# Optimization experiments

Hardware: AMD Instinct MI355X
Metric: run time of the kernel (lower is better)

## Reference

```python
import jax, jax.numpy as jnp
import numpy as np

DIM = 384
HEADS = 12
WS = 7
MLPH = 1536
B = 32
EPS = 1e-5


def _rel_index():
    coords = np.stack(np.meshgrid(np.arange(WS), np.arange(WS), indexing='ij'))  # [2,7,7]
    cf = coords.reshape(2, -1)  # [2,49]
    rel = cf[:, :, None] - cf[:, None, :]  # [2,49,49]
    rel = rel.transpose(1, 2, 0).astype(np.int64)
    rel[:, :, 0] += WS - 1
    rel[:, :, 1] += WS - 1
    rel[:, :, 0] *= 2 * WS - 1
    return jnp.asarray(rel.sum(-1), dtype=jnp.int32)  # [49,49]


def setup_inputs() -> dict:
    key = jax.random.key(0)
    ks = jax.random.split(key, 16)
    H, W = 56, 56
    L = H * W
    s = 0.02
    inp = {
        'x': jax.random.normal(ks[0], (B, L, DIM), jnp.float32),
        'ln1_g': jnp.ones((DIM,), jnp.float32),
        'ln1_b': jnp.zeros((DIM,), jnp.float32),
        'qkv_w': jax.random.normal(ks[1], (DIM, 3 * DIM), jnp.float32) * s,
        'qkv_b': jnp.zeros((3 * DIM,), jnp.float32),
        'rpb_table': jax.random.normal(ks[2], ((2 * WS - 1) ** 2, HEADS), jnp.float32) * s,
        'proj_w': jax.random.normal(ks[3], (DIM, DIM), jnp.float32) * s,
        'proj_b': jnp.zeros((DIM,), jnp.float32),
        'ln2_g': jnp.ones((DIM,), jnp.float32),
        'ln2_b': jnp.zeros((DIM,), jnp.float32),
        'mlp_w1': jax.random.normal(ks[4], (DIM, MLPH), jnp.float32) * s,
        'mlp_b1': jnp.zeros((MLPH,), jnp.float32),
        'mlp_w2': jax.random.normal(ks[5], (MLPH, DIM), jnp.float32) * s,
        'mlp_b2': jnp.zeros((DIM,), jnp.float32),
        'rel_idx': _rel_index(),
        'H': H,
        'W': W,
    }
    return inp


def _ln(x, g, b):
    m = jnp.mean(x, axis=-1, keepdims=True)
    v = jnp.mean(jnp.square(x - m), axis=-1, keepdims=True)
    return (x - m) * jax.lax.rsqrt(v + EPS) * g + b


def reference(x, ln1_g, ln1_b, qkv_w, qkv_b, rpb_table, proj_w, proj_b,
              ln2_g, ln2_b, mlp_w1, mlp_b1, mlp_w2, mlp_b2, rel_idx, H, W):
    Bb, L, C = x.shape
    N = WS * WS
    hd = C // HEADS
    scale = hd ** -0.5

    shortcut = x
    h = _ln(x, ln1_g, ln1_b).reshape(Bb, H, W, C)
    # window partition -> [nW, 49, C]
    h = h.reshape(Bb, H // WS, WS, W // WS, WS, C).transpose(0, 1, 3, 2, 4, 5)
    wins = h.reshape(-1, N, C)
    nW = wins.shape[0]

    qkv = (wins @ qkv_w + qkv_b).reshape(nW, N, 3, HEADS, hd).transpose(2, 0, 3, 1, 4)
    q, k, v = qkv[0] * scale, qkv[1], qkv[2]  # [nW, heads, 49, hd]

    attn = jnp.einsum('bhnd,bhmd->bhnm', q, k)
    bias = rpb_table[rel_idx].transpose(2, 0, 1)  # [heads,49,49]
    attn = jax.nn.softmax(attn + bias[None], axis=-1)
    out = jnp.einsum('bhnm,bhmd->bhnd', attn, v).transpose(0, 2, 1, 3).reshape(nW, N, C)
    out = out @ proj_w + proj_b

    # window reverse -> [B, L, C]
    out = out.reshape(Bb, H // WS, W // WS, WS, WS, C).transpose(0, 1, 3, 2, 4, 5).reshape(Bb, L, C)

    x = shortcut + out
    h2 = _ln(x, ln2_g, ln2_b)
    mlp = jax.nn.gelu(h2 @ mlp_w1 + mlp_b1, approximate=False) @ mlp_w2 + mlp_b2
    return x + mlp
```

## Files before the change

kernel.cpp:

```cpp
#include <hip/hip_runtime.h>
#include <hip/hip_bf16.h>
#include <cstdint>
#include <cstddef>

#define HEADS 12
#define LL 3136
#define ROWS 100352
#define SCALE 0.17677669529663687f

typedef __hip_bfloat16 bf16;
typedef __attribute__((ext_vector_type(8))) short short8;
typedef __attribute__((ext_vector_type(4))) short s4;
typedef __attribute__((ext_vector_type(4))) float f32x4;

__device__ __forceinline__ float bf2f(unsigned short u) {
  union { uint32_t u32; float f; } x; x.u32 = ((uint32_t)u) << 16; return x.f;
}
__device__ __forceinline__ unsigned short f2bf_bits(float f) {
  union { float f; uint32_t u; } x; x.f = f;
  uint32_t r = x.u + 0x7fffu + ((x.u >> 16) & 1u);
  return (unsigned short)(r >> 16);
}

__global__ void prep_transpose(const float* __restrict__ src, bf16* __restrict__ dst,
                               int K, int N, int scaleLim, float scale) {
  int idx = blockIdx.x * 256 + threadIdx.x;
  if (idx >= K * N) return;
  int n = idx / K;
  int k = idx - n * K;
  float v = src[(size_t)k * N + n];
  if (n < scaleLim) v *= scale;
  dst[idx] = __float2bfloat16(v);
}

__global__ void prep_qb(const float* __restrict__ qkv_b, float* __restrict__ qb) {
  int idx = blockIdx.x * 256 + threadIdx.x;
  if (idx < 1152) qb[idx] = qkv_b[idx] * (idx < 384 ? SCALE : 1.0f);
}

__global__ void prep_biasM(const float* __restrict__ rpb, const int* __restrict__ rel,
                           f32x4* __restrict__ biasM) {
  int h = blockIdx.x;
  int t = blockIdx.y;
  int mi = t >> 2, ni = t & 3;
  int lane = threadIdx.x;
  int q = ni * 16 + (lane & 15);
  int g = lane >> 4;
  f32x4 v;
  #pragma unroll
  for (int j = 0; j < 4; ++j) {
    int k = mi * 16 + g * 4 + j;
    float b;
    if (k < 49) b = (q < 49) ? rpb[rel[q * 49 + k] * HEADS + h] : 0.f;
    else        b = -1e30f;
    v[j] = b;
  }
  biasM[((h * 4 + mi) * 4 + ni) * 64 + lane] = v;
}

template<bool WIN>
__global__ __launch_bounds__(256) void ln_kernel(const float* __restrict__ x,
    const float* __restrict__ g, const float* __restrict__ b, bf16* __restrict__ out) {
  int row = blockIdx.x * 4 + (threadIdx.x >> 6);
  int lane = threadIdx.x & 63;
  size_t src;
  if (WIN) {
    int w = row / 49, p = row - w * 49;
    int bb = w >> 6, wy = (w >> 3) & 7, wx = w & 7;
    int iy = p / 7, ix = p - iy * 7;
    int l = (wy * 7 + iy) * 56 + wx * 7 + ix;
    src = ((size_t)bb * LL + l) * 384;
  } else {
    src = (size_t)row * 384;
  }
  const float* xr = x + src;
  float vals[6];
  float s = 0.f, s2 = 0.f;
  #pragma unroll
  for (int j = 0; j < 6; ++j) {
    float v = xr[lane + 64 * j];
    vals[j] = v; s += v; s2 += v * v;
  }
  #pragma unroll
  for (int off = 32; off >= 1; off >>= 1) {
    s  += __shfl_xor(s, off);
    s2 += __shfl_xor(s2, off);
  }
  float m  = s * (1.f / 384.f);
  float var = s2 * (1.f / 384.f) - m * m;
  float rs = rsqrtf(var + 1e-5f);
  bf16* orow = out + (size_t)row * 384;
  #pragma unroll
  for (int j = 0; j < 6; ++j) {
    int c = lane + 64 * j;
    orow[c] = __float2bfloat16((vals[j] - m) * rs * g[c] + b[c]);
  }
}

template<int EPI>
__global__ __launch_bounds__(256) void gemm_bt(const bf16* __restrict__ A,
    const bf16* __restrict__ Bt, const float* __restrict__ bias,
    bf16* __restrict__ Cb, float* __restrict__ Cf, const float* __restrict__ resid,
    int M, int N, int K) {
  __shared__ bf16 lsA[2][128 * 32];
  __shared__ bf16 lsB[2][128 * 32];
  const int t = threadIdx.x;
  const int lane = t & 63;
  const int wave = t >> 6;
  const int wm = wave >> 1, wn = wave & 1;
  const int lrow = lane & 15;
  const int lk = (lane >> 4) * 8;
  const int n0 = blockIdx.x * 128;
  const int m0 = blockIdx.y * 128;

  f32x4 acc[4][4];
  #pragma unroll
  for (int i = 0; i < 4; ++i)
    #pragma unroll
    for (int j = 0; j < 4; ++j) acc[i][j] = (f32x4){0.f, 0.f, 0.f, 0.f};

  auto stage = [&](int buf, int k0) {
    #pragma unroll
    for (int i = 0; i < 2; ++i) {
      int e = (i * 256 + t) * 8;
      int r = e >> 5, c = e & 31;
      const bf16* ga = A  + (size_t)(m0 + r) * K + (k0 + c);
      const bf16* gb = Bt + (size_t)(n0 + r) * K + (k0 + c);
      __builtin_amdgcn_global_load_lds((const __attribute__((address_space(1))) void*)ga,
          (__attribute__((address_space(3))) void*)&lsA[buf][e], 16, 0, 0);
      __builtin_amdgcn_global_load_lds((const __attribute__((address_space(1))) void*)gb,
          (__attribute__((address_space(3))) void*)&lsB[buf][e], 16, 0, 0);
    }
  };

  auto compute = [&](int buf) {
    short8 af[4], bfr[4];
    #pragma unroll
    for (int mi = 0; mi < 4; ++mi)
      af[mi] = *(const short8*)&lsA[buf][(wm * 64 + mi * 16 + lrow) * 32 + lk];
    #pragma unroll
    for (int ni = 0; ni < 4; ++ni)
      bfr[ni] = *(const short8*)&lsB[buf][(wn * 64 + ni * 16 + lrow) * 32 + lk];
    #pragma unroll
    for (int mi = 0; mi < 4; ++mi)
      #pragma unroll
      for (int ni = 0; ni < 4; ++ni)
        acc[mi][ni] = __builtin_amdgcn_mfma_f32_16x16x32_bf16(af[mi], bfr[ni], acc[mi][ni], 0, 0, 0);
  };

  stage(0, 0);
  __syncthreads();
  int cur = 0;
  const int nt = K >> 5;
  for (int it = 0; it < nt - 1; ++it) {
    stage(cur ^ 1, (it + 1) * 32);
    compute(cur);
    __syncthreads();
    cur ^= 1;
  }
  compute(cur);

  #pragma unroll
  for (int mi = 0; mi < 4; ++mi) {
    #pragma unroll
    for (int ni = 0; ni < 4; ++ni) {
      int col = n0 + wn * 64 + ni * 16 + lrow;
      float bv = bias[col];
      #pragma unroll
      for (int j = 0; j < 4; ++j) {
        int row = m0 + wm * 64 + mi * 16 + (lane >> 4) * 4 + j;
        float v = acc[mi][ni][j] + bv;
        if constexpr (EPI == 0) {
          Cb[(size_t)row * N + col] = __float2bfloat16(v);
        } else if constexpr (EPI == 1) {
          v = v * 0.5f * (1.0f + erff(v * 0.70710678118654752f));
          Cb[(size_t)row * N + col] = __float2bfloat16(v);
        } else if constexpr (EPI == 2) {
          int w = row / 49, p = row - w * 49;
          int bb = w >> 6, wy = (w >> 3) & 7, wx = w & 7;
          int iy = p / 7, ix = p - iy * 7;
          int l = (wy * 7 + iy) * 56 + wx * 7 + ix;
          size_t di = ((size_t)bb * LL + l) * 384 + col;
          Cf[di] = v + resid[di];
        } else {
          size_t di = (size_t)row * N + col;
          Cf[di] = v + resid[di];
        }
      }
    }
  }
}

__global__ __launch_bounds__(256) void attn_mfma(const bf16* __restrict__ qkv,
    const f32x4* __restrict__ biasM, bf16* __restrict__ out) {
  __shared__ __align__(16) short lds4[4][6272];
  const int wv = threadIdx.x >> 6;
  const int lane = threadIdx.x & 63;
  const int w = blockIdx.x * 4 + wv;
  const int h = blockIdx.y;
  short* L = &lds4[wv][0];
  const short* base = (const short*)(qkv + (size_t)w * 49 * 1152 + h * 32);

  #pragma unroll
  for (int i = 0; i < 4; ++i) {
    int t = i * 64 + lane;
    int r = t >> 2, c = t & 3;
    short8 qv, kv, vv;
    if (r < 49) {
      const short* rp = base + (size_t)r * 1152;
      qv = *(const short8*)(rp + c * 8);
      kv = *(const short8*)(rp + 384 + c * 8);
      vv = *(const short8*)(rp + 768 + c * 8);
    } else {
      qv = (short8)0; kv = (short8)0; vv = (short8)0;
    }
    *(short8*)&L[r * 32 + c * 8] = kv;
    *(short8*)&L[2048 + r * 32 + c * 8] = qv;
    #pragma unroll
    for (int j = 0; j < 8; ++j) L[4096 + (c * 8 + j) * 68 + r] = vv[j];
  }

  const int g = lane >> 4, r15 = lane & 15;

  short8 ka[4], qb[4];
  #pragma unroll
  for (int mi = 0; mi < 4; ++mi)
    ka[mi] = *(const short8*)&L[(mi * 16 + r15) * 32 + g * 8];
  #pragma unroll
  for (int ni = 0; ni < 4; ++ni)
    qb[ni] = *(const short8*)&L[2048 + (ni * 16 + r15) * 32 + g * 8];

  f32x4 sT[4][4];
  #pragma unroll
  for (int mi = 0; mi < 4; ++mi)
    #pragma unroll
    for (int ni = 0; ni < 4; ++ni)
      sT[mi][ni] = biasM[((h * 4 + mi) * 4 + ni) * 64 + lane];
  #pragma unroll
  for (int mi = 0; mi < 4; ++mi)
    #pragma unroll
    for (int ni = 0; ni < 4; ++ni)
      sT[mi][ni] = __builtin_amdgcn_mfma_f32_16x16x32_bf16(ka[mi], qb[ni], sT[mi][ni], 0, 0, 0);

  float inv_[4];
  #pragma unroll
  for (int ni = 0; ni < 4; ++ni) {
    float m = -1e30f;
    #pragma unroll
    for (int mi = 0; mi < 4; ++mi)
      #pragma unroll
      for (int j = 0; j < 4; ++j) m = fmaxf(m, sT[mi][ni][j]);
    m = fmaxf(m, __shfl_xor(m, 16));
    m = fmaxf(m, __shfl_xor(m, 32));
    float s = 0.f;
    #pragma unroll
    for (int mi = 0; mi < 4; ++mi)
      #pragma unroll
      for (int j = 0; j < 4; ++j) {
        float p = __expf(sT[mi][ni][j] - m);
        sT[mi][ni][j] = p; s += p;
      }
    s += __shfl_xor(s, 16);
    s += __shfl_xor(s, 32);
    inv_[ni] = 1.f / s;
  }

  s4 pa[4][4];
  #pragma unroll
  for (int mi = 0; mi < 4; ++mi)
    #pragma unroll
    for (int ni = 0; ni < 4; ++ni) {
      s4 p;
      #pragma unroll
      for (int j = 0; j < 4; ++j)
        p[j] = (short)f2bf_bits(sT[mi][ni][j] * inv_[ni]);
      pa[mi][ni] = p;
    }

  s4 vb[4][2];
  #pragma unroll
  for (int mi = 0; mi < 4; ++mi)
    #pragma unroll
    for (int di = 0; di < 2; ++di)
      vb[mi][di] = *(const s4*)&L[4096 + (di * 16 + r15) * 68 + mi * 16 + g * 4];

  f32x4 o[4][2];
  #pragma unroll
  for (int ni = 0; ni < 4; ++ni)
    #pragma unroll
    for (int di = 0; di < 2; ++di) o[ni][di] = (f32x4){0.f, 0.f, 0.f, 0.f};

  asm volatile("s_nop 3" ::: );
  #pragma unroll
  for (int ni = 0; ni < 4; ++ni)
    #pragma unroll
    for (int di = 0; di < 2; ++di)
      #pragma unroll
      for (int mi = 0; mi < 4; ++mi) {
#if __has_builtin(__builtin_amdgcn_mfma_f32_16x16x16bf16_1k)
        o[ni][di] = __builtin_amdgcn_mfma_f32_16x16x16bf16_1k(pa[mi][ni], vb[mi][di], o[ni][di], 0, 0, 0);
#else
        asm volatile("v_mfma_f32_16x16x16_bf16 %0, %1, %2, %0"
                     : "+v"(o[ni][di]) : "v"(pa[mi][ni]), "v"(vb[mi][di]));
#endif
      }
  asm volatile("s_nop 7\n\ts_nop 7" ::: );

  bf16* op = out + ((size_t)w * 49) * 384 + h * 32;
  #pragma unroll
  for (int ni = 0; ni < 4; ++ni)
    #pragma unroll
    for (int di = 0; di < 2; ++di)
      #pragma unroll
      for (int j = 0; j < 4; ++j) {
        int q = ni * 16 + g * 4 + j;
        if (q < 49)
          op[(size_t)q * 384 + di * 16 + r15] = __float2bfloat16(o[ni][di][j]);
      }
}

extern "C" void kernel_launch(void* const* d_in, const int* in_sizes, int n_in,
                              void* d_out, int out_size, void* d_ws, size_t ws_size,
                              hipStream_t stream) {
  const float* x      = (const float*)d_in[0];
  const float* ln1_g  = (const float*)d_in[1];
  const float* ln1_b  = (const float*)d_in[2];
  const float* qkv_w  = (const float*)d_in[3];
  const float* qkv_b  = (const float*)d_in[4];
  const float* rpb    = (const float*)d_in[5];
  const float* proj_w = (const float*)d_in[6];
  const float* proj_b = (const float*)d_in[7];
  const float* ln2_g  = (const float*)d_in[8];
  const float* ln2_b  = (const float*)d_in[9];
  const float* mlp_w1 = (const float*)d_in[10];
  const float* mlp_b1 = (const float*)d_in[11];
  const float* mlp_w2 = (const float*)d_in[12];
  const float* mlp_b2 = (const float*)d_in[13];
  const int*   rel    = (const int*)d_in[14];

  char* ws = (char*)d_ws;
  const size_t OFF_WQKV  = 0;
  const size_t OFF_WPROJ = OFF_WQKV + (size_t)1152 * 384 * 2;
  const size_t OFF_WM1   = OFF_WPROJ + (size_t)384 * 384 * 2;
  const size_t OFF_WM2   = OFF_WM1 + (size_t)1536 * 384 * 2;
  const size_t OFF_QB    = OFF_WM2 + (size_t)384 * 1536 * 2;
  const size_t OFF_HWIN  = 3659776;
  const size_t OFF_QKV   = OFF_HWIN + (size_t)ROWS * 384 * 2;
  const size_t OFF_ATTN  = OFF_QKV + (size_t)ROWS * 1152 * 2;
  const size_t OFF_X2    = OFF_ATTN + (size_t)ROWS * 384 * 2;
  const size_t OFF_M1    = OFF_QKV;
  const size_t OFF_H2    = OFF_HWIN;
  const size_t OFF_BIASM = OFF_X2;

  bf16*  wqkv  = (bf16*)(ws + OFF_WQKV);
  bf16*  wproj = (bf16*)(ws + OFF_WPROJ);
  bf16*  wm1   = (bf16*)(ws + OFF_WM1);
  bf16*  wm2   = (bf16*)(ws + OFF_WM2);
  float* qb    = (float*)(ws + OFF_QB);
  f32x4* biasM = (f32x4*)(ws + OFF_BIASM);
  bf16*  hwin  = (bf16*)(ws + OFF_HWIN);
  bf16*  qkvb  = (bf16*)(ws + OFF_QKV);
  bf16*  attnb = (bf16*)(ws + OFF_ATTN);
  float* x2    = (float*)(ws + OFF_X2);
  bf16*  m1    = (bf16*)(ws + OFF_M1);
  bf16*  h2    = (bf16*)(ws + OFF_H2);
  float* outp  = (float*)d_out;

  prep_transpose<<<(384 * 1152 + 255) / 256, 256, 0, stream>>>(qkv_w, wqkv, 384, 1152, 384, SCALE);
  prep_transpose<<<(384 * 384 + 255) / 256, 256, 0, stream>>>(proj_w, wproj, 384, 384, 0, 1.f);
  prep_transpose<<<(384 * 1536 + 255) / 256, 256, 0, stream>>>(mlp_w1, wm1, 384, 1536, 0, 1.f);
  prep_transpose<<<(1536 * 384 + 255) / 256, 256, 0, stream>>>(mlp_w2, wm2, 1536, 384, 0, 1.f);
  prep_qb<<<5, 256, 0, stream>>>(qkv_b, qb);
  prep_biasM<<<dim3(12, 16), 64, 0, stream>>>(rpb, rel, biasM);

  ln_kernel<true><<<ROWS / 4, 256, 0, stream>>>(x, ln1_g, ln1_b, hwin);
  gemm_bt<0><<<dim3(1152 / 128, ROWS / 128), 256, 0, stream>>>(
      hwin, wqkv, qb, qkvb, nullptr, nullptr, ROWS, 1152, 384);
  attn_mfma<<<dim3(512, HEADS), 256, 0, stream>>>(qkvb, biasM, attnb);
  gemm_bt<2><<<dim3(384 / 128, ROWS / 128), 256, 0, stream>>>(
      attnb, wproj, proj_b, nullptr, x2, x, ROWS, 384, 384);
  ln_kernel<false><<<ROWS / 4, 256, 0, stream>>>(x2, ln2_g, ln2_b, h2);
  gemm_bt<1><<<dim3(1536 / 128, ROWS / 128), 256, 0, stream>>>(
      h2, wm1, mlp_b1, m1, nullptr, nullptr, ROWS, 1536, 384);
  gemm_bt<3><<<dim3(384 / 128, ROWS / 128), 256, 0, stream>>>(
      m1, wm2, mlp_b2, nullptr, outp, x2, ROWS, 384, 1536);
}
```

Measured before the change: 951.2 us.

## Triple-buffer GEMM K-loop with vmcnt waits and tile the weight transpose

The GEMM main loop moves from double to triple buffering in LDS. It prefetches two K-tiles ahead and uses explicit s_waitcnt vmcnt plus raw barriers, so global-to-LDS loads overlap more with MFMA work. Separately, the weight prep transpose now goes through a shared-memory 64x64 tile so both reads and writes are coalesced. Triple buffering raises LDS use per block, which may reduce occupancy, and the hand-coded vmcnt counts depend on the number of loads each thread issues.

```diff
diff --git a/kernel.cpp b/kernel.cpp
--- a/kernel.cpp
+++ b/kernel.cpp
@@ -22,15 +22,25 @@
   return (unsigned short)(r >> 16);
 }
 
-__global__ void prep_transpose(const float* __restrict__ src, bf16* __restrict__ dst,
-                               int K, int N, int scaleLim, float scale) {
-  int idx = blockIdx.x * 256 + threadIdx.x;
-  if (idx >= K * N) return;
-  int n = idx / K;
-  int k = idx - n * K;
-  float v = src[(size_t)k * N + n];
-  if (n < scaleLim) v *= scale;
-  dst[idx] = __float2bfloat16(v);
+__global__ __launch_bounds__(256) void prep_transpose(const float* __restrict__ src,
+    bf16* __restrict__ dst, int K, int N, int scaleLim, float scale) {
+  __shared__ float tile[64][65];
+  const int kb = blockIdx.x * 64, nb = blockIdx.y * 64;
+  const int tx = threadIdx.x & 63;
+  const int ty = threadIdx.x >> 6;
+  #pragma unroll
+  for (int i = 0; i < 16; ++i) {
+    int k = ty * 16 + i;
+    tile[k][tx] = src[(size_t)(kb + k) * N + nb + tx];
+  }
+  __syncthreads();
+  #pragma unroll
+  for (int i = 0; i < 16; ++i) {
+    int n = ty * 16 + i;
+    float v = tile[tx][n];
+    if (nb + n < scaleLim) v *= scale;
+    dst[(size_t)(nb + n) * K + kb + tx] = __float2bfloat16(v);
+  }
 }
 
 __global__ void prep_qb(const float* __restrict__ qkv_b, float* __restrict__ qb) {
@@ -102,8 +112,8 @@
     const bf16* __restrict__ Bt, const float* __restrict__ bias,
     bf16* __restrict__ Cb, float* __restrict__ Cf, const float* __restrict__ resid,
     int M, int N, int K) {
-  __shared__ bf16 lsA[2][128 * 32];
-  __shared__ bf16 lsB[2][128 * 32];
+  __shared__ bf16 lsA[3][128 * 32];
+  __shared__ bf16 lsB[3][128 * 32];
   const int t = threadIdx.x;
   const int lane = t & 63;
   const int wave = t >> 6;
@@ -119,7 +129,8 @@
     #pragma unroll
     for (int j = 0; j < 4; ++j) acc[i][j] = (f32x4){0.f, 0.f, 0.f, 0.f};
 
-  auto stage = [&](int buf, int k0) {
+  auto stage = [&](int buf, int tile) {
+    int k0 = tile * 32;
     #pragma unroll
     for (int i = 0; i < 2; ++i) {
       int e = (i * 256 + t) * 8;
@@ -148,17 +159,22 @@
         acc[mi][ni] = __builtin_amdgcn_mfma_f32_16x16x32_bf16(af[mi], bfr[ni], acc[mi][ni], 0, 0, 0);
   };
 
+  const int nt = K >> 5;
   stage(0, 0);
-  __syncthreads();
-  int cur = 0;
-  const int nt = K >> 5;
-  for (int it = 0; it < nt - 1; ++it) {
-    stage(cur ^ 1, (it + 1) * 32);
+  if (nt > 1) stage(1, 1);
+  int cur = 0, pre = 2;
+  for (int it = 0; it < nt; ++it) {
+    __builtin_amdgcn_s_barrier();
+    if (it + 2 < nt) stage(pre, it + 2);
+    int rem = nt - 1 - it;
+    if (rem >= 2)      asm volatile("s_waitcnt vmcnt(8)" ::: "memory");
+    else if (rem == 1) asm volatile("s_waitcnt vmcnt(4)" ::: "memory");
+    else               asm volatile("s_waitcnt vmcnt(0)" ::: "memory");
+    __builtin_amdgcn_s_barrier();
     compute(cur);
-    __syncthreads();
-    cur ^= 1;
-  }
-  compute(cur);
+    pre = cur;
+    cur = (cur == 2) ? 0 : cur + 1;
+  }
 
   #pragma unroll
   for (int mi = 0; mi < 4; ++mi) {
@@ -366,10 +382,10 @@
   bf16*  h2    = (bf16*)(ws + OFF_H2);
   float* outp  = (float*)d_out;
 
-  prep_transpose<<<(384 * 1152 + 255) / 256, 256, 0, stream>>>(qkv_w, wqkv, 384, 1152, 384, SCALE);
-  prep_transpose<<<(384 * 384 + 255) / 256, 256, 0, stream>>>(proj_w, wproj, 384, 384, 0, 1.f);
-  prep_transpose<<<(384 * 1536 + 255) / 256, 256, 0, stream>>>(mlp_w1, wm1, 384, 1536, 0, 1.f);
-  prep_transpose<<<(1536 * 384 + 255) / 256, 256, 0, stream>>>(mlp_w2, wm2, 1536, 384, 0, 1.f);
+  prep_transpose<<<dim3(384 / 64, 1152 / 64), 256, 0, stream>>>(qkv_w, wqkv, 384, 1152, 384, SCALE);
+  prep_transpose<<<dim3(384 / 64, 384 / 64), 256, 0, stream>>>(proj_w, wproj, 384, 384, 0, 1.f);
+  prep_transpose<<<dim3(384 / 64, 1536 / 64), 256, 0, stream>>>(mlp_w1, wm1, 384, 1536, 0, 1.f);
+  prep_transpose<<<dim3(1536 / 64, 384 / 64), 256, 0, stream>>>(mlp_w2, wm2, 1536, 384, 0, 1.f);
   prep_qb<<<5, 256, 0, stream>>>(qkv_b, qb);
   prep_biasM<<<dim3(12, 16), 64, 0, stream>>>(rpb, rel, biasM);
 
```

After: 960.7 us. Within noise of the previous version (+1.0%).
